# Optimization experiments

Hardware: AMD Instinct MI355X
Metric: run time of the kernel (lower is better)

The kernel has to match this reference:

```python
import jax, jax.numpy as jnp
import numpy as np

N_NODES = 100000


def setup_inputs() -> dict:
    key = jax.random.key(0)
    k1, k2, k3, k4 = jax.random.split(key, 4)
    x = jax.random.normal(k1, (N_NODES, 64), dtype=jnp.float32)
    W = jax.random.normal(k2, (64, 64), dtype=jnp.float32) * (1.0 / np.sqrt(64.0))
    src = jax.random.randint(k3, (1600000,), 0, N_NODES, dtype=jnp.int32)
    dst = jax.random.randint(k4, (1600000,), 0, N_NODES, dtype=jnp.int32)
    return {"x": x, "W": W, "src": src, "dst": dst}


def reference(x, W, src, dst):
    n = x.shape[0]
    ones = jnp.ones(src.shape[0], dtype=x.dtype)
    out_deg = jax.ops.segment_sum(ones, src, num_segments=n)  # out-degree of each node
    in_deg = jax.ops.segment_sum(ones, dst, num_segments=n)   # in-degree of each node
    norm_src = jnp.power(jnp.clip(out_deg, 1.0, None), -0.5)  # D_out^{-1/2}, clamp(min=1)
    norm_dst = jnp.power(jnp.clip(in_deg, 1.0, None), -0.5)   # D_in^{-1/2}, clamp(min=1)
    # in_feats == out_feats -> DGL aggregates first, then applies the weight
    feat = x * norm_src[:, None]                              # [N, d_in]
    msgs = feat[src]                                          # [E, d_in] gather
    agg = jax.ops.segment_sum(msgs, dst, num_segments=n)      # [N, d_in] scatter-add
    agg = agg * norm_dst[:, None]
    return agg @ W                                            # [N, d_out]
```

## Files before the change

### kernel.cpp

```cpp
#include <hip/hip_runtime.h>
#include <math.h>

#define D 64
#define SCAN_TILE 1024
#define SCAN_THREADS 256
#define SCAN_ITEMS 4
#define HS 16
#define BSHIFT 9
#define BW 512
#define CHUNK 8192

__device__ __forceinline__ unsigned pack_bf16(float a, float b) {
    unsigned ua = __float_as_uint(a);
    unsigned ub = __float_as_uint(b);
    ua = (ua + 0x7fffu + ((ua >> 16) & 1u)) >> 16;
    ub = (ub + 0x7fffu + ((ub >> 16) & 1u)) >> 16;
    return ua | (ub << 16);
}
__device__ __forceinline__ float blo(unsigned u) { return __uint_as_float(u << 16); }
__device__ __forceinline__ float bhi(unsigned u) { return __uint_as_float(u & 0xffff0000u); }


__global__ __launch_bounds__(256)
void bucket_count_chunks2_kernel(const int* __restrict__ src, const int* __restrict__ dst,
                                 int* __restrict__ bcnt_d, int* __restrict__ bcnt_s,
                                 int E, int NBv) {
    __shared__ int cd[256];
    __shared__ int cs[256];
    for (int i = threadIdx.x; i < NBv; i += 256) { cd[i] = 0; cs[i] = 0; }
    __syncthreads();
    int beg = blockIdx.x * CHUNK;
    int end = beg + CHUNK; if (end > E) end = E;
    for (int j = beg + threadIdx.x; j < end; j += 256) {
        atomicAdd(&cd[dst[j] >> BSHIFT], 1);
        atomicAdd(&cs[src[j] >> BSHIFT], 1);
    }
    __syncthreads();
    for (int i = threadIdx.x; i < NBv; i += 256) {
        bcnt_d[(size_t)blockIdx.x * NBv + i] = cd[i];
        bcnt_s[(size_t)blockIdx.x * NBv + i] = cs[i];
    }
}

__global__ __launch_bounds__(256)
void bucket_scan_chunks2_kernel(const int* __restrict__ bcnt_d, int* __restrict__ bstart_d,
                                int* __restrict__ btot_d,
                                const int* __restrict__ bcnt_s, int* __restrict__ bstart_s,
                                int* __restrict__ btot_s,
                                int nChunks, int NBv) {
    __shared__ int sdata[256];
    int which = (blockIdx.x >= NBv) ? 1 : 0;
    int b = blockIdx.x - which * NBv;
    const int* bcnt   = which ? bcnt_s : bcnt_d;
    int*       bstart = which ? bstart_s : bstart_d;
    int*       btot   = which ? btot_s : btot_d;
    int t = threadIdx.x;
    int carry = 0;
    for (int c0 = 0; c0 < nChunks; c0 += 256) {
        int c = c0 + t;
        int v = (c < nChunks) ? bcnt[(size_t)c * NBv + b] : 0;
        sdata[t] = v;
        __syncthreads();
        for (int off = 1; off < 256; off <<= 1) {
            int val = (t >= off) ? sdata[t - off] : 0;
            __syncthreads();
            if (t >= off) sdata[t] += val;
            __syncthreads();
        }
        if (c < nChunks) bstart[(size_t)c * NBv + b] = carry + sdata[t] - v;
        carry += sdata[255];
        __syncthreads();
    }
    if (t == 0) btot[b] = carry;
}

__global__ __launch_bounds__(256)
void bucket_base2_kernel(const int* __restrict__ btot_d, int* __restrict__ bbeg_d,
                         const int* __restrict__ btot_s, int* __restrict__ bbeg_s,
                         int NBv, int E) {
    __shared__ int sdata[256];
    const int* btot = (blockIdx.x == 0) ? btot_d : btot_s;
    int*       bbeg = (blockIdx.x == 0) ? bbeg_d : bbeg_s;
    int t = threadIdx.x;
    int v = (t < NBv) ? btot[t] : 0;
    sdata[t] = v;
    __syncthreads();
    for (int off = 1; off < 256; off <<= 1) {
        int val = (t >= off) ? sdata[t - off] : 0;
        __syncthreads();
        if (t >= off) sdata[t] += val;
        __syncthreads();
    }
    if (t < NBv) bbeg[t] = sdata[t] - v;
    if (t == 0) bbeg[NBv] = E;
}

__global__ __launch_bounds__(256)
void bucket_scatter2_kernel(const int* __restrict__ src, const int* __restrict__ dst,
                            const int* __restrict__ bstart_d, const int* __restrict__ bbeg_d,
                            const int* __restrict__ bstart_s, const int* __restrict__ bbeg_s,
                            unsigned* __restrict__ bucketed_d,
                            unsigned short* __restrict__ bucketed_s,
                            int E, int NBv) {
    __shared__ int cur_d[256];
    __shared__ int cur_s[256];
    for (int i = threadIdx.x; i < NBv; i += 256) {
        cur_d[i] = bstart_d[(size_t)blockIdx.x * NBv + i] + bbeg_d[i];
        cur_s[i] = bstart_s[(size_t)blockIdx.x * NBv + i] + bbeg_s[i];
    }
    __syncthreads();
    int beg = blockIdx.x * CHUNK;
    int end = beg + CHUNK; if (end > E) end = E;
    for (int j = beg + threadIdx.x; j < end; j += 256) {
        int d = dst[j];
        int s = src[j];
        int pd = atomicAdd(&cur_d[d >> BSHIFT], 1);
        bucketed_d[pd] = ((unsigned)(d & (BW - 1)) << 17) | (unsigned)s;
        int ps = atomicAdd(&cur_s[s >> BSHIFT], 1);
        bucketed_s[ps] = (unsigned short)(s & (BW - 1));
    }
}

__global__ __launch_bounds__(256)
void bucket_count_dst_kernel(const unsigned* __restrict__ bucketed_d,
                             const int* __restrict__ bbeg_d, int* __restrict__ cnt_dst,
                             float* __restrict__ norm_dst, int N) {
    __shared__ int cnt[BW];
    int b = blockIdx.x;
    for (int i = threadIdx.x; i < BW; i += 256) cnt[i] = 0;
    __syncthreads();
    int beg = bbeg_d[b], end = bbeg_d[b + 1];
    for (int j = beg + threadIdx.x; j < end; j += 256) {
        atomicAdd(&cnt[bucketed_d[j] >> 17], 1);
    }
    __syncthreads();
    int dbase = b << BSHIFT;
    for (int i = threadIdx.x; i < BW; i += 256) {
        int d = dbase + i;
        if (d < N) {
            int c = cnt[i];
            cnt_dst[d] = c;
            norm_dst[d] = 1.0f / sqrtf((float)(c < 1 ? 1 : c));
        }
    }
}

__global__ __launch_bounds__(256)
void bucket_count_src_kernel(const unsigned short* __restrict__ bucketed_s,
                             const int* __restrict__ bbeg_s, float* __restrict__ norm_src,
                             int N) {
    __shared__ int cnt[BW];
    int b = blockIdx.x;
    for (int i = threadIdx.x; i < BW; i += 256) cnt[i] = 0;
    __syncthreads();
    int beg = bbeg_s[b], end = bbeg_s[b + 1];
    for (int j = beg + threadIdx.x; j < end; j += 256) {
        atomicAdd(&cnt[bucketed_s[j]], 1);
    }
    __syncthreads();
    int sbase = b << BSHIFT;
    for (int i = threadIdx.x; i < BW; i += 256) {
        int s = sbase + i;
        if (s < N) {
            int c = cnt[i];
            norm_src[s] = 1.0f / sqrtf((float)(c < 1 ? 1 : c));
        }
    }
}

__global__ __launch_bounds__(256)
void bucket_place_kernel(const unsigned* __restrict__ bucketed_d,
                         const int* __restrict__ bbeg_d, const int* __restrict__ offsets,
                         int* __restrict__ sorted_src, int N) {
    __shared__ int cur[BW];
    int b = blockIdx.x;
    int dbase = b << BSHIFT;
    for (int i = threadIdx.x; i < BW; i += 256) {
        int d = dbase + i;
        cur[i] = (d < N) ? offsets[d] : 0;
    }
    __syncthreads();
    int beg = bbeg_d[b], end = bbeg_d[b + 1];
    for (int j = beg + threadIdx.x; j < end; j += 256) {
        unsigned v = bucketed_d[j];
        int pos = atomicAdd(&cur[v >> 17], 1);
        sorted_src[pos] = (int)(v & 0x1FFFFu);
    }
}


__global__ __launch_bounds__(SCAN_THREADS)
void scan_blocks_kernel(const int* __restrict__ cnt_dst, int* __restrict__ offsets,
                        int* __restrict__ partials, int N, int S) {
    __shared__ int sdata[SCAN_THREADS];
    int t = threadIdx.x;
    int base = blockIdx.x * SCAN_TILE + t * SCAN_ITEMS;
    int v[SCAN_ITEMS];
    int sum = 0;
    #pragma unroll
    for (int i = 0; i < SCAN_ITEMS; ++i) {
        int idx = base + i;
        v[i] = (idx < N) ? cnt_dst[(size_t)idx * S] : 0;
        sum += v[i];
    }
    sdata[t] = sum;
    __syncthreads();
    for (int off = 1; off < SCAN_THREADS; off <<= 1) {
        int val = (t >= off) ? sdata[t - off] : 0;
        __syncthreads();
        if (t >= off) sdata[t] += val;
        __syncthreads();
    }
    int excl = sdata[t] - sum;
    if (t == SCAN_THREADS - 1) partials[blockIdx.x] = sdata[t];
    int run = excl;
    #pragma unroll
    for (int i = 0; i < SCAN_ITEMS; ++i) {
        int idx = base + i;
        if (idx < N) offsets[idx] = run;
        run += v[i];
    }
}

__global__ __launch_bounds__(SCAN_THREADS)
void scan_partials_kernel(int* __restrict__ partials, int nblk) {
    __shared__ int sdata[SCAN_THREADS];
    int t = threadIdx.x;
    int v = (t < nblk) ? partials[t] : 0;
    sdata[t] = v;
    __syncthreads();
    for (int off = 1; off < SCAN_THREADS; off <<= 1) {
        int val = (t >= off) ? sdata[t - off] : 0;
        __syncthreads();
        if (t >= off) sdata[t] += val;
        __syncthreads();
    }
    if (t < nblk) partials[t] = sdata[t] - v;
}

__global__ void add_back2_kernel(int* __restrict__ offsets, const int* __restrict__ partials,
                                 int N, int E) {
    int i = blockIdx.x * blockDim.x + threadIdx.x;
    if (i < N) offsets[i] += partials[i >> 10];
    if (i == 0) offsets[N] = E;
}

__global__ void add_back_kernel(int* __restrict__ offsets, int* __restrict__ cursor,
                                const int* __restrict__ partials, int N, int E, int S) {
    int i = blockIdx.x * blockDim.x + threadIdx.x;
    if (i < N) {
        int o = offsets[i] + partials[i >> 10];
        offsets[i] = o;
        cursor[(size_t)i * S] = o;
    }
    if (i == 0) offsets[N] = E;
}


#define XW_ROWS 64
#define ATP 68

__global__ __launch_bounds__(256, 4)
void xw_tiled_kernel(const float4* __restrict__ x4, const float* __restrict__ W,
                     const float* __restrict__ norm_src, unsigned* __restrict__ y, int N) {
    __shared__ float Ws[D * D];
    __shared__ float At[D][ATP];
    int t = threadIdx.x;

    for (int i = t; i < D * D / 4; i += 256)
        reinterpret_cast<float4*>(Ws)[i] = reinterpret_cast<const float4*>(W)[i];

    int rowbase = blockIdx.x * XW_ROWS;
    int lr = t >> 2;
    int qc = t & 3;
    int gr = rowbase + lr;
    float ns = (gr < N) ? norm_src[gr] : 0.0f;
    #pragma unroll
    for (int c = qc; c < 16; c += 4) {
        float4 v = (gr < N) ? x4[(size_t)gr * 16 + c] : make_float4(0.f, 0.f, 0.f, 0.f);
        At[c * 4 + 0][lr] = v.x * ns;
        At[c * 4 + 1][lr] = v.y * ns;
        At[c * 4 + 2][lr] = v.z * ns;
        At[c * 4 + 3][lr] = v.w * ns;
    }
    __syncthreads();

    int tx = t & 15;
    int ty = t >> 4;
    float4 acc0 = make_float4(0.f, 0.f, 0.f, 0.f);
    float4 acc1 = acc0, acc2 = acc0, acc3 = acc0;
    #pragma unroll 4
    for (int k = 0; k < D; ++k) {
        float4 a = *reinterpret_cast<const float4*>(&At[k][ty * 4]);
        float4 w = *reinterpret_cast<const float4*>(&Ws[k * D + tx * 4]);
        acc0.x += a.x * w.x; acc0.y += a.x * w.y; acc0.z += a.x * w.z; acc0.w += a.x * w.w;
        acc1.x += a.y * w.x; acc1.y += a.y * w.y; acc1.z += a.y * w.z; acc1.w += a.y * w.w;
        acc2.x += a.z * w.x; acc2.y += a.z * w.y; acc2.z += a.z * w.z; acc2.w += a.z * w.w;
        acc3.x += a.w * w.x; acc3.y += a.w * w.y; acc3.z += a.w * w.z; acc3.w += a.w * w.w;
    }

    uint2* y2 = reinterpret_cast<uint2*>(y);
    int r0 = rowbase + ty * 4;
    if (r0 + 0 < N) y2[(size_t)(r0 + 0) * 16 + tx] =
        make_uint2(pack_bf16(acc0.x, acc0.y), pack_bf16(acc0.z, acc0.w));
    if (r0 + 1 < N) y2[(size_t)(r0 + 1) * 16 + tx] =
        make_uint2(pack_bf16(acc1.x, acc1.y), pack_bf16(acc1.z, acc1.w));
    if (r0 + 2 < N) y2[(size_t)(r0 + 2) * 16 + tx] =
        make_uint2(pack_bf16(acc2.x, acc2.y), pack_bf16(acc2.z, acc2.w));
    if (r0 + 3 < N) y2[(size_t)(r0 + 3) * 16 + tx] =
        make_uint2(pack_bf16(acc3.x, acc3.y), pack_bf16(acc3.z, acc3.w));
}


__global__ __launch_bounds__(256)
void agg_bf16_kernel(const uint4* __restrict__ y4, const int* __restrict__ offsets,
                     const int* __restrict__ sorted_src, const float* __restrict__ norm_dst,
                     float4* __restrict__ out4, int N) {
    int wave = (blockIdx.x << 2) + (threadIdx.x >> 6);
    if (wave >= N) return;
    int lane = threadIdx.x & 63;
    int g = lane >> 3;
    int q = lane & 7;
    int beg = offsets[wave];
    int end = offsets[wave + 1];
    float nd = norm_dst[wave];
    float a0 = 0.f, a1 = 0.f, a2 = 0.f, a3 = 0.f, a4 = 0.f, a5 = 0.f, a6 = 0.f, a7 = 0.f;
    int j = beg + g;
    while (j + 8 < end) {
        int s0 = sorted_src[j];
        int s1 = sorted_src[j + 8];
        uint4 v0 = y4[(size_t)s0 * 8 + q];
        uint4 v1 = y4[(size_t)s1 * 8 + q];
        a0 += blo(v0.x) + blo(v1.x); a1 += bhi(v0.x) + bhi(v1.x);
        a2 += blo(v0.y) + blo(v1.y); a3 += bhi(v0.y) + bhi(v1.y);
        a4 += blo(v0.z) + blo(v1.z); a5 += bhi(v0.z) + bhi(v1.z);
        a6 += blo(v0.w) + blo(v1.w); a7 += bhi(v0.w) + bhi(v1.w);
        j += 16;
    }
    if (j < end) {
        int s = sorted_src[j];
        uint4 v = y4[(size_t)s * 8 + q];
        a0 += blo(v.x); a1 += bhi(v.x);
        a2 += blo(v.y); a3 += bhi(v.y);
        a4 += blo(v.z); a5 += bhi(v.z);
        a6 += blo(v.w); a7 += bhi(v.w);
    }
    a0 += __shfl_xor(a0, 8);  a1 += __shfl_xor(a1, 8);
    a2 += __shfl_xor(a2, 8);  a3 += __shfl_xor(a3, 8);
    a4 += __shfl_xor(a4, 8);  a5 += __shfl_xor(a5, 8);
    a6 += __shfl_xor(a6, 8);  a7 += __shfl_xor(a7, 8);
    a0 += __shfl_xor(a0, 16); a1 += __shfl_xor(a1, 16);
    a2 += __shfl_xor(a2, 16); a3 += __shfl_xor(a3, 16);
    a4 += __shfl_xor(a4, 16); a5 += __shfl_xor(a5, 16);
    a6 += __shfl_xor(a6, 16); a7 += __shfl_xor(a7, 16);
    a0 += __shfl_xor(a0, 32); a1 += __shfl_xor(a1, 32);
    a2 += __shfl_xor(a2, 32); a3 += __shfl_xor(a3, 32);
    a4 += __shfl_xor(a4, 32); a5 += __shfl_xor(a5, 32);
    a6 += __shfl_xor(a6, 32); a7 += __shfl_xor(a7, 32);
    if (lane < 8) {
        float4 o1; o1.x = a0 * nd; o1.y = a1 * nd; o1.z = a2 * nd; o1.w = a3 * nd;
        float4 o2; o2.x = a4 * nd; o2.y = a5 * nd; o2.z = a6 * nd; o2.w = a7 * nd;
        out4[(size_t)wave * 16 + q * 2]     = o1;
        out4[(size_t)wave * 16 + q * 2 + 1] = o2;
    }
}


__global__ void hist4_kernel(const int* __restrict__ src, const int* __restrict__ dst,
                             int* __restrict__ cnt, int E, int N, int S) {
    int i = blockIdx.x * blockDim.x + threadIdx.x;
    int E4 = E >> 2;
    if (i < E4) {
        int4 s = reinterpret_cast<const int4*>(src)[i];
        int4 d = reinterpret_cast<const int4*>(dst)[i];
        atomicAdd(&cnt[s.x * S], 1); atomicAdd(&cnt[s.y * S], 1);
        atomicAdd(&cnt[s.z * S], 1); atomicAdd(&cnt[s.w * S], 1);
        atomicAdd(&cnt[(N + d.x) * S], 1); atomicAdd(&cnt[(N + d.y) * S], 1);
        atomicAdd(&cnt[(N + d.z) * S], 1); atomicAdd(&cnt[(N + d.w) * S], 1);
    }
    if (i == 0) {
        for (int e = E4 << 2; e < E; ++e) {
            atomicAdd(&cnt[src[e] * S], 1);
            atomicAdd(&cnt[(N + dst[e]) * S], 1);
        }
    }
}

__global__ void norm_from_cnt_kernel(const int* __restrict__ cnt, float* __restrict__ norm,
                                     int twoN, int S) {
    int i = blockIdx.x * blockDim.x + threadIdx.x;
    if (i < twoN) {
        int c = cnt[(size_t)i * S];
        float v = (float)(c < 1 ? 1 : c);
        norm[i] = 1.0f / sqrtf(v);
    }
}

__global__ void bin4_kernel(const int* __restrict__ src, const int* __restrict__ dst,
                            int* __restrict__ cursor, int* __restrict__ sorted_src,
                            int E, int S) {
    int i = blockIdx.x * blockDim.x + threadIdx.x;
    int E4 = E >> 2;
    if (i < E4) {
        int4 s = reinterpret_cast<const int4*>(src)[i];
        int4 d = reinterpret_cast<const int4*>(dst)[i];
        sorted_src[atomicAdd(&cursor[d.x * S], 1)] = s.x;
        sorted_src[atomicAdd(&cursor[d.y * S], 1)] = s.y;
        sorted_src[atomicAdd(&cursor[d.z * S], 1)] = s.z;
        sorted_src[atomicAdd(&cursor[d.w * S], 1)] = s.w;
    }
    if (i == 0) {
        for (int e = E4 << 2; e < E; ++e) {
            sorted_src[atomicAdd(&cursor[dst[e] * S], 1)] = src[e];
        }
    }
}

__global__ void deg_kernel(const int* __restrict__ src, const int* __restrict__ dst,
                           float* __restrict__ deg, int E, int N) {
    int i = blockIdx.x * blockDim.x + threadIdx.x;
    if (i < E) {
        atomicAdd(&deg[src[i]], 1.0f);
        atomicAdd(&deg[N + dst[i]], 1.0f);
    }
}

__global__ void norm_kernel(float* __restrict__ deg, int twoN) {
    int i = blockIdx.x * blockDim.x + threadIdx.x;
    if (i < twoN) {
        float v = deg[i];
        v = v < 1.0f ? 1.0f : v;
        deg[i] = 1.0f / sqrtf(v);
    }
}

__global__ void scatter_kernel(const float* __restrict__ x, const int* __restrict__ src,
                               const int* __restrict__ dst, const float* __restrict__ norm_src,
                               float* __restrict__ agg, int E) {
    int tid = blockIdx.x * blockDim.x + threadIdx.x;
    int e = tid >> 4;
    int q = tid & 15;
    if (e < E) {
        int s = src[e];
        int d = dst[e];
        float ns = norm_src[s];
        float4 v = reinterpret_cast<const float4*>(x)[s * (D / 4) + q];
        float* o = agg + (long long)d * D + q * 4;
        atomicAdd(o + 0, v.x * ns);
        atomicAdd(o + 1, v.y * ns);
        atomicAdd(o + 2, v.z * ns);
        atomicAdd(o + 3, v.w * ns);
    }
}

__global__ __launch_bounds__(256) void gemm_kernel(float* __restrict__ out,
                                                   const float* __restrict__ W,
                                                   const float* __restrict__ norm_dst,
                                                   int N, int rows_per_block) {
    __shared__ float Ws[D * D];
    __shared__ float rowS[4][D];
    for (int i = threadIdx.x; i < D * D; i += 256) Ws[i] = W[i];

    int f   = threadIdx.x & 63;
    int sub = threadIdx.x >> 6;
    int base = blockIdx.x * rows_per_block;

    for (int r0 = 0; r0 < rows_per_block; r0 += 4) {
        int r = base + r0 + sub;
        bool valid = (r < N);
        __syncthreads();
        if (valid) rowS[sub][f] = out[(long long)r * D + f] * norm_dst[r];
        __syncthreads();
        if (valid) {
            float acc = 0.0f;
            #pragma unroll
            for (int k = 0; k < D; ++k) acc += rowS[sub][k] * Ws[k * D + f];
            out[(long long)r * D + f] = acc;
        }
    }
}

extern "C" void kernel_launch(void* const* d_in, const int* in_sizes, int n_in,
                              void* d_out, int out_size, void* d_ws, size_t ws_size,
                              hipStream_t stream) {
    const float* x   = (const float*)d_in[0];
    const float* W   = (const float*)d_in[1];
    const int*   src = (const int*)d_in[2];
    const int*   dst = (const int*)d_in[3];

    const int N = in_sizes[0] / D;
    const int E = in_sizes[2];
    const int nblk = (N + SCAN_TILE - 1) / SCAN_TILE;
    const int NBv = (N + BW - 1) >> BSHIFT;
    const int nChunks = (E + CHUNK - 1) / CHUNK;

    size_t w_norm = 0;
    size_t w_cntd = w_norm + 2 * (size_t)N;
    size_t w_offs = w_cntd + (size_t)N;
    size_t w_part = w_offs + (size_t)N + 1;
    size_t w_bcd  = w_part + SCAN_THREADS;
    size_t w_bsd  = w_bcd + (size_t)nChunks * NBv;
    size_t w_bcs  = w_bsd + (size_t)nChunks * NBv;
    size_t w_bss  = w_bcs + (size_t)nChunks * NBv;
    size_t w_btd  = w_bss + (size_t)nChunks * NBv;
    size_t w_bbd  = w_btd + (size_t)NBv;
    size_t w_bts  = w_bbd + (size_t)NBv + 1;
    size_t w_bbs  = w_bts + (size_t)NBv;
    size_t w_bkd  = w_bbs + (size_t)NBv + 1;
    size_t w_bks  = w_bkd + (size_t)E;
    size_t w_sort = w_bks + ((size_t)E + 1) / 2;
    size_t w_y    = (w_sort + (size_t)E + 3) & ~(size_t)3;
    size_t need_new = (w_y + (size_t)N * 32) * 4;

    bool new_ok = (N <= (1 << 17)) && (NBv <= 256) && (nblk <= SCAN_THREADS) &&
                  (ws_size >= need_new);

    if (new_ok) {
        float*          norm       = (float*)d_ws + w_norm;
        int*            cnt_dst    = (int*)d_ws + w_cntd;
        int*            offsets    = (int*)d_ws + w_offs;
        int*            partials   = (int*)d_ws + w_part;
        int*            bcnt_d     = (int*)d_ws + w_bcd;
        int*            bstart_d   = (int*)d_ws + w_bsd;
        int*            bcnt_s     = (int*)d_ws + w_bcs;
        int*            bstart_s   = (int*)d_ws + w_bss;
        int*            btot_d     = (int*)d_ws + w_btd;
        int*            bbeg_d     = (int*)d_ws + w_bbd;
        int*            btot_s     = (int*)d_ws + w_bts;
        int*            bbeg_s     = (int*)d_ws + w_bbs;
        unsigned*       bucketed_d = (unsigned*)d_ws + w_bkd;
        unsigned short* bucketed_s = (unsigned short*)((int*)d_ws + w_bks);
        int*            sorted_src = (int*)d_ws + w_sort;
        unsigned*       y          = (unsigned*)d_ws + w_y;
        float*          out        = (float*)d_out;

        bucket_count_chunks2_kernel<<<nChunks, 256, 0, stream>>>(src, dst, bcnt_d, bcnt_s,
                                                                 E, NBv);
        bucket_scan_chunks2_kernel<<<2 * NBv, 256, 0, stream>>>(bcnt_d, bstart_d, btot_d,
                                                                bcnt_s, bstart_s, btot_s,
                                                                nChunks, NBv);
        bucket_base2_kernel<<<2, 256, 0, stream>>>(btot_d, bbeg_d, btot_s, bbeg_s, NBv, E);
        bucket_scatter2_kernel<<<nChunks, 256, 0, stream>>>(src, dst, bstart_d, bbeg_d,
                                                            bstart_s, bbeg_s, bucketed_d,
                                                            bucketed_s, E, NBv);
        bucket_count_src_kernel<<<NBv, 256, 0, stream>>>(bucketed_s, bbeg_s, norm, N);
        bucket_count_dst_kernel<<<NBv, 256, 0, stream>>>(bucketed_d, bbeg_d, cnt_dst,
                                                         norm + N, N);

        scan_blocks_kernel<<<nblk, SCAN_THREADS, 0, stream>>>(cnt_dst, offsets, partials, N, 1);
        scan_partials_kernel<<<1, SCAN_THREADS, 0, stream>>>(partials, nblk);
        add_back2_kernel<<<(N + 255) / 256, 256, 0, stream>>>(offsets, partials, N, E);

        bucket_place_kernel<<<NBv, 256, 0, stream>>>(bucketed_d, bbeg_d, offsets,
                                                     sorted_src, N);

        xw_tiled_kernel<<<(N + XW_ROWS - 1) / XW_ROWS, 256, 0, stream>>>(
            (const float4*)x, W, norm, y, N);
        int agg_blocks = (N + 3) / 4;
        agg_bf16_kernel<<<agg_blocks, 256, 0, stream>>>(
            (const uint4*)y, offsets, sorted_src, norm + N, (float4*)out, N);
        return;
    }

    {
        const int strides[4] = {16, 8, 4, 1};
        int S = 0;
        size_t o_norm = 0, o_cnt = 0, o_offs = 0, o_cur = 0, o_part = 0, o_sort = 0, o_yy = 0;
        size_t need_A = 0;
        for (int t = 0; t < 4; ++t) {
            int s = strides[t];
            o_norm = 0;
            o_cnt  = o_norm + 2 * (size_t)N;
            o_offs = o_cnt + 2 * (size_t)N * s;
            o_cur  = o_offs + (size_t)N + 1;
            o_part = o_cur + (size_t)N * s;
            o_sort = o_part + SCAN_THREADS;
            o_yy   = (o_sort + (size_t)E + 3) & ~(size_t)3;
            need_A = (o_yy + (size_t)N * 32) * 4;
            if (ws_size >= need_A) { S = s; break; }
        }
        if (S > 0 && nblk <= SCAN_THREADS) {
            float*    norm       = (float*)d_ws + o_norm;
            int*      cnt        = (int*)d_ws + o_cnt;
            int*      offsets    = (int*)d_ws + o_offs;
            int*      cursor     = (int*)d_ws + o_cur;
            int*      partials   = (int*)d_ws + o_part;
            int*      sorted_src = (int*)d_ws + o_sort;
            unsigned* y          = (unsigned*)d_ws + o_yy;
            float*    out        = (float*)d_out;

            hipMemsetAsync(cnt, 0, 2 * (size_t)N * S * sizeof(int), stream);

            int E4 = E >> 2;
            int histblk = (E4 + 255) / 256; if (histblk < 1) histblk = 1;
            hist4_kernel<<<histblk, 256, 0, stream>>>(src, dst, cnt, E, N, S);
            norm_from_cnt_kernel<<<(2 * N + 255) / 256, 256, 0, stream>>>(cnt, norm, 2 * N, S);
            scan_blocks_kernel<<<nblk, SCAN_THREADS, 0, stream>>>(cnt + (size_t)N * S, offsets,
                                                                  partials, N, S);
            scan_partials_kernel<<<1, SCAN_THREADS, 0, stream>>>(partials, nblk);
            add_back_kernel<<<(N + 255) / 256, 256, 0, stream>>>(offsets, cursor, partials,
                                                                 N, E, S);
            bin4_kernel<<<histblk, 256, 0, stream>>>(src, dst, cursor, sorted_src, E, S);

            xw_tiled_kernel<<<(N + XW_ROWS - 1) / XW_ROWS, 256, 0, stream>>>(
                (const float4*)x, W, norm, y, N);
            int agg_blocks = (N + 3) / 4;
            agg_bf16_kernel<<<agg_blocks, 256, 0, stream>>>(
                (const uint4*)y, offsets, sorted_src, norm + N, (float4*)out, N);
            return;
        }
    }

    {
        float* deg = (float*)d_ws;
        float* agg = (float*)d_out;

        hipMemsetAsync(deg, 0, (size_t)2 * N * sizeof(float), stream);
        hipMemsetAsync(agg, 0, (size_t)N * D * sizeof(float), stream);

        deg_kernel<<<(E + 255) / 256, 256, 0, stream>>>(src, dst, deg, E, N);
        norm_kernel<<<(2 * N + 255) / 256, 256, 0, stream>>>(deg, 2 * N);

        long long scatter_threads = (long long)E * 16;
        int scatter_blocks = (int)((scatter_threads + 255) / 256);
        scatter_kernel<<<scatter_blocks, 256, 0, stream>>>(x, src, dst, deg, agg, E);

        const int rows_per_block = 64;
        int gemm_blocks = (N + rows_per_block - 1) / rows_per_block;
        gemm_kernel<<<gemm_blocks, 256, 0, stream>>>(agg, W, deg + N, N, rows_per_block);
    }
}
```

Baseline: 155.2 us.

## Map eight lanes per destination row in aggregation instead of one wave

The aggregation kernel now gives each destination row 8 lanes (each loading one 16-byte bf16 slice), so a wave covers 8 rows instead of one. Each lane walks that row's edges serially, unrolled by 4, and the cross-lane shuffle reduction goes away. With about 16 edges per row, the old mapping left most lanes idle or needed a shuffle reduction at the end. In exchange, each lane runs a longer serial edge loop, and rows of different degree in the same wave cause divergence.

```diff
diff --git a/kernel.cpp b/kernel.cpp
--- a/kernel.cpp
+++ b/kernel.cpp
@@ -316,26 +316,43 @@
 void agg_bf16_kernel(const uint4* __restrict__ y4, const int* __restrict__ offsets,
                      const int* __restrict__ sorted_src, const float* __restrict__ norm_dst,
                      float4* __restrict__ out4, int N) {
-    int wave = (blockIdx.x << 2) + (threadIdx.x >> 6);
-    if (wave >= N) return;
-    int lane = threadIdx.x & 63;
-    int g = lane >> 3;
-    int q = lane & 7;
-    int beg = offsets[wave];
-    int end = offsets[wave + 1];
-    float nd = norm_dst[wave];
+    int row = blockIdx.x * 32 + (threadIdx.x >> 3);
+    if (row >= N) return;
+    int q = threadIdx.x & 7;
+    int beg = offsets[row];
+    int end = offsets[row + 1];
+    float nd = norm_dst[row];
     float a0 = 0.f, a1 = 0.f, a2 = 0.f, a3 = 0.f, a4 = 0.f, a5 = 0.f, a6 = 0.f, a7 = 0.f;
-    int j = beg + g;
-    while (j + 8 < end) {
+    int j = beg;
+    while (j + 3 < end) {
         int s0 = sorted_src[j];
-        int s1 = sorted_src[j + 8];
+        int s1 = sorted_src[j + 1];
+        int s2 = sorted_src[j + 2];
+        int s3 = sorted_src[j + 3];
+        uint4 v0 = y4[(size_t)s0 * 8 + q];
+        uint4 v1 = y4[(size_t)s1 * 8 + q];
+        uint4 v2 = y4[(size_t)s2 * 8 + q];
+        uint4 v3 = y4[(size_t)s3 * 8 + q];
+        a0 += (blo(v0.x) + blo(v1.x)) + (blo(v2.x) + blo(v3.x));
+        a1 += (bhi(v0.x) + bhi(v1.x)) + (bhi(v2.x) + bhi(v3.x));
+        a2 += (blo(v0.y) + blo(v1.y)) + (blo(v2.y) + blo(v3.y));
+        a3 += (bhi(v0.y) + bhi(v1.y)) + (bhi(v2.y) + bhi(v3.y));
+        a4 += (blo(v0.z) + blo(v1.z)) + (blo(v2.z) + blo(v3.z));
+        a5 += (bhi(v0.z) + bhi(v1.z)) + (bhi(v2.z) + bhi(v3.z));
+        a6 += (blo(v0.w) + blo(v1.w)) + (blo(v2.w) + blo(v3.w));
+        a7 += (bhi(v0.w) + bhi(v1.w)) + (bhi(v2.w) + bhi(v3.w));
+        j += 4;
+    }
+    if (j + 1 < end) {
+        int s0 = sorted_src[j];
+        int s1 = sorted_src[j + 1];
         uint4 v0 = y4[(size_t)s0 * 8 + q];
         uint4 v1 = y4[(size_t)s1 * 8 + q];
         a0 += blo(v0.x) + blo(v1.x); a1 += bhi(v0.x) + bhi(v1.x);
         a2 += blo(v0.y) + blo(v1.y); a3 += bhi(v0.y) + bhi(v1.y);
         a4 += blo(v0.z) + blo(v1.z); a5 += bhi(v0.z) + bhi(v1.z);
         a6 += blo(v0.w) + blo(v1.w); a7 += bhi(v0.w) + bhi(v1.w);
-        j += 16;
+        j += 2;
     }
     if (j < end) {
         int s = sorted_src[j];
@@ -345,24 +362,10 @@
         a4 += blo(v.z); a5 += bhi(v.z);
         a6 += blo(v.w); a7 += bhi(v.w);
     }
-    a0 += __shfl_xor(a0, 8);  a1 += __shfl_xor(a1, 8);
-    a2 += __shfl_xor(a2, 8);  a3 += __shfl_xor(a3, 8);
-    a4 += __shfl_xor(a4, 8);  a5 += __shfl_xor(a5, 8);
-    a6 += __shfl_xor(a6, 8);  a7 += __shfl_xor(a7, 8);
-    a0 += __shfl_xor(a0, 16); a1 += __shfl_xor(a1, 16);
-    a2 += __shfl_xor(a2, 16); a3 += __shfl_xor(a3, 16);
-    a4 += __shfl_xor(a4, 16); a5 += __shfl_xor(a5, 16);
-    a6 += __shfl_xor(a6, 16); a7 += __shfl_xor(a7, 16);
-    a0 += __shfl_xor(a0, 32); a1 += __shfl_xor(a1, 32);
-    a2 += __shfl_xor(a2, 32); a3 += __shfl_xor(a3, 32);
-    a4 += __shfl_xor(a4, 32); a5 += __shfl_xor(a5, 32);
-    a6 += __shfl_xor(a6, 32); a7 += __shfl_xor(a7, 32);
-    if (lane < 8) {
-        float4 o1; o1.x = a0 * nd; o1.y = a1 * nd; o1.z = a2 * nd; o1.w = a3 * nd;
-        float4 o2; o2.x = a4 * nd; o2.y = a5 * nd; o2.z = a6 * nd; o2.w = a7 * nd;
-        out4[(size_t)wave * 16 + q * 2]     = o1;
-        out4[(size_t)wave * 16 + q * 2 + 1] = o2;
-    }
+    float4 o1; o1.x = a0 * nd; o1.y = a1 * nd; o1.z = a2 * nd; o1.w = a3 * nd;
+    float4 o2; o2.x = a4 * nd; o2.y = a5 * nd; o2.z = a6 * nd; o2.w = a7 * nd;
+    out4[(size_t)row * 16 + q * 2]     = o1;
+    out4[(size_t)row * 16 + q * 2 + 1] = o2;
 }
 
 
@@ -556,7 +559,7 @@
 
         xw_tiled_kernel<<<(N + XW_ROWS - 1) / XW_ROWS, 256, 0, stream>>>(
             (const float4*)x, W, norm, y, N);
-        int agg_blocks = (N + 3) / 4;
+        int agg_blocks = (N + 31) / 32;
         agg_bf16_kernel<<<agg_blocks, 256, 0, stream>>>(
             (const uint4*)y, offsets, sorted_src, norm + N, (float4*)out, N);
         return;
@@ -604,7 +607,7 @@
 
             xw_tiled_kernel<<<(N + XW_ROWS - 1) / XW_ROWS, 256, 0, stream>>>(
                 (const float4*)x, W, norm, y, N);
-            int agg_blocks = (N + 3) / 4;
+            int agg_blocks = (N + 31) / 32;
             agg_bf16_kernel<<<agg_blocks, 256, 0, stream>>>(
                 (const uint4*)y, offsets, sorted_src, norm + N, (float4*)out, N);
             return;
```

Measured after the change: 157.3 us. Within noise of the previous version (+1.4%).

## Fuse degree count, CSR offset scan and placement into one bucket kernel

Applied to the files above, without the earlier changes.

Replaces the separate src/dst count kernels, the three-kernel global prefix scan, and the placement kernel with a single finalize kernel. Because buckets are already laid out contiguously by destination range, each block derives its node offsets from the bucket base plus a local block scan, so no global scan is needed. It also shrinks CHUNK from 8192 to 2048 to give the count and scatter stages more blocks. This cuts five kernel launches and one global pass over the counts, but grows the per-chunk bucket count tables and the bucket-scan work.

```diff
diff --git a/kernel.cpp b/kernel.cpp
--- a/kernel.cpp
+++ b/kernel.cpp
@@ -8,7 +8,7 @@
 #define HS 16
 #define BSHIFT 9
 #define BW 512
-#define CHUNK 8192
+#define CHUNK 2048
 
 __device__ __forceinline__ unsigned pack_bf16(float a, float b) {
     unsigned ua = __float_as_uint(a);
@@ -122,69 +122,71 @@
 }
 
 __global__ __launch_bounds__(256)
-void bucket_count_dst_kernel(const unsigned* __restrict__ bucketed_d,
-                             const int* __restrict__ bbeg_d, int* __restrict__ cnt_dst,
-                             float* __restrict__ norm_dst, int N) {
+void bucket_finalize_kernel(const unsigned* __restrict__ bucketed_d,
+                            const int* __restrict__ bbeg_d,
+                            const unsigned short* __restrict__ bucketed_s,
+                            const int* __restrict__ bbeg_s,
+                            int* __restrict__ offsets, float* __restrict__ norm_dst,
+                            float* __restrict__ norm_src, int* __restrict__ sorted_src,
+                            int N, int E, int NBv) {
     __shared__ int cnt[BW];
-    int b = blockIdx.x;
-    for (int i = threadIdx.x; i < BW; i += 256) cnt[i] = 0;
-    __syncthreads();
-    int beg = bbeg_d[b], end = bbeg_d[b + 1];
-    for (int j = beg + threadIdx.x; j < end; j += 256) {
-        atomicAdd(&cnt[bucketed_d[j] >> 17], 1);
-    }
-    __syncthreads();
-    int dbase = b << BSHIFT;
-    for (int i = threadIdx.x; i < BW; i += 256) {
-        int d = dbase + i;
-        if (d < N) {
-            int c = cnt[i];
-            cnt_dst[d] = c;
-            norm_dst[d] = 1.0f / sqrtf((float)(c < 1 ? 1 : c));
-        }
-    }
-}
-
-__global__ __launch_bounds__(256)
-void bucket_count_src_kernel(const unsigned short* __restrict__ bucketed_s,
-                             const int* __restrict__ bbeg_s, float* __restrict__ norm_src,
-                             int N) {
-    __shared__ int cnt[BW];
-    int b = blockIdx.x;
-    for (int i = threadIdx.x; i < BW; i += 256) cnt[i] = 0;
-    __syncthreads();
-    int beg = bbeg_s[b], end = bbeg_s[b + 1];
-    for (int j = beg + threadIdx.x; j < end; j += 256) {
-        atomicAdd(&cnt[bucketed_s[j]], 1);
-    }
-    __syncthreads();
-    int sbase = b << BSHIFT;
-    for (int i = threadIdx.x; i < BW; i += 256) {
-        int s = sbase + i;
-        if (s < N) {
-            int c = cnt[i];
-            norm_src[s] = 1.0f / sqrtf((float)(c < 1 ? 1 : c));
-        }
-    }
-}
-
-__global__ __launch_bounds__(256)
-void bucket_place_kernel(const unsigned* __restrict__ bucketed_d,
-                         const int* __restrict__ bbeg_d, const int* __restrict__ offsets,
-                         int* __restrict__ sorted_src, int N) {
     __shared__ int cur[BW];
-    int b = blockIdx.x;
-    int dbase = b << BSHIFT;
-    for (int i = threadIdx.x; i < BW; i += 256) {
-        int d = dbase + i;
-        cur[i] = (d < N) ? offsets[d] : 0;
-    }
-    __syncthreads();
-    int beg = bbeg_d[b], end = bbeg_d[b + 1];
-    for (int j = beg + threadIdx.x; j < end; j += 256) {
-        unsigned v = bucketed_d[j];
-        int pos = atomicAdd(&cur[v >> 17], 1);
-        sorted_src[pos] = (int)(v & 0x1FFFFu);
+    __shared__ int ssum[256];
+    int t = threadIdx.x;
+    if (blockIdx.x < NBv) {
+        int b = blockIdx.x;
+        cnt[t] = 0; cnt[t + 256] = 0;
+        __syncthreads();
+        int beg = bbeg_d[b], end = bbeg_d[b + 1];
+        for (int j = beg + t; j < end; j += 256)
+            atomicAdd(&cnt[bucketed_d[j] >> 17], 1);
+        __syncthreads();
+        int c0 = cnt[2 * t], c1 = cnt[2 * t + 1];
+        ssum[t] = c0 + c1;
+        __syncthreads();
+        for (int off = 1; off < 256; off <<= 1) {
+            int v = (t >= off) ? ssum[t - off] : 0;
+            __syncthreads();
+            if (t >= off) ssum[t] += v;
+            __syncthreads();
+        }
+        int excl = ssum[t] - (c0 + c1);
+        int off0 = beg + excl;
+        int off1 = off0 + c0;
+        int dbase = b << BSHIFT;
+        int d0 = dbase + 2 * t, d1 = dbase + 2 * t + 1;
+        cur[2 * t] = off0; cur[2 * t + 1] = off1;
+        if (d0 < N) {
+            offsets[d0] = off0;
+            norm_dst[d0] = 1.0f / sqrtf((float)(c0 < 1 ? 1 : c0));
+        }
+        if (d1 < N) {
+            offsets[d1] = off1;
+            norm_dst[d1] = 1.0f / sqrtf((float)(c1 < 1 ? 1 : c1));
+        }
+        if (b == NBv - 1 && t == 0) offsets[N] = E;
+        __syncthreads();
+        for (int j = beg + t; j < end; j += 256) {
+            unsigned v = bucketed_d[j];
+            int pos = atomicAdd(&cur[v >> 17], 1);
+            sorted_src[pos] = (int)(v & 0x1FFFFu);
+        }
+    } else {
+        int b = blockIdx.x - NBv;
+        cnt[t] = 0; cnt[t + 256] = 0;
+        __syncthreads();
+        int beg = bbeg_s[b], end = bbeg_s[b + 1];
+        for (int j = beg + t; j < end; j += 256)
+            atomicAdd(&cnt[bucketed_s[j]], 1);
+        __syncthreads();
+        int sbase = b << BSHIFT;
+        for (int i = t; i < BW; i += 256) {
+            int s = sbase + i;
+            if (s < N) {
+                int c = cnt[i];
+                norm_src[s] = 1.0f / sqrtf((float)(c < 1 ? 1 : c));
+            }
+        }
     }
 }
 
@@ -236,13 +238,6 @@
         __syncthreads();
     }
     if (t < nblk) partials[t] = sdata[t] - v;
-}
-
-__global__ void add_back2_kernel(int* __restrict__ offsets, const int* __restrict__ partials,
-                                 int N, int E) {
-    int i = blockIdx.x * blockDim.x + threadIdx.x;
-    if (i < N) offsets[i] += partials[i >> 10];
-    if (i == 0) offsets[N] = E;
 }
 
 __global__ void add_back_kernel(int* __restrict__ offsets, int* __restrict__ cursor,
@@ -495,10 +490,8 @@
     const int nChunks = (E + CHUNK - 1) / CHUNK;
 
     size_t w_norm = 0;
-    size_t w_cntd = w_norm + 2 * (size_t)N;
-    size_t w_offs = w_cntd + (size_t)N;
-    size_t w_part = w_offs + (size_t)N + 1;
-    size_t w_bcd  = w_part + SCAN_THREADS;
+    size_t w_offs = w_norm + 2 * (size_t)N;
+    size_t w_bcd  = w_offs + (size_t)N + 1;
     size_t w_bsd  = w_bcd + (size_t)nChunks * NBv;
     size_t w_bcs  = w_bsd + (size_t)nChunks * NBv;
     size_t w_bss  = w_bcs + (size_t)nChunks * NBv;
@@ -512,14 +505,11 @@
     size_t w_y    = (w_sort + (size_t)E + 3) & ~(size_t)3;
     size_t need_new = (w_y + (size_t)N * 32) * 4;
 
-    bool new_ok = (N <= (1 << 17)) && (NBv <= 256) && (nblk <= SCAN_THREADS) &&
-                  (ws_size >= need_new);
+    bool new_ok = (N <= (1 << 17)) && (NBv <= 256) && (ws_size >= need_new);
 
     if (new_ok) {
         float*          norm       = (float*)d_ws + w_norm;
-        int*            cnt_dst    = (int*)d_ws + w_cntd;
         int*            offsets    = (int*)d_ws + w_offs;
-        int*            partials   = (int*)d_ws + w_part;
         int*            bcnt_d     = (int*)d_ws + w_bcd;
         int*            bstart_d   = (int*)d_ws + w_bsd;
         int*            bcnt_s     = (int*)d_ws + w_bcs;
@@ -543,16 +533,10 @@
         bucket_scatter2_kernel<<<nChunks, 256, 0, stream>>>(src, dst, bstart_d, bbeg_d,
                                                             bstart_s, bbeg_s, bucketed_d,
                                                             bucketed_s, E, NBv);
-        bucket_count_src_kernel<<<NBv, 256, 0, stream>>>(bucketed_s, bbeg_s, norm, N);
-        bucket_count_dst_kernel<<<NBv, 256, 0, stream>>>(bucketed_d, bbeg_d, cnt_dst,
-                                                         norm + N, N);
-
-        scan_blocks_kernel<<<nblk, SCAN_THREADS, 0, stream>>>(cnt_dst, offsets, partials, N, 1);
-        scan_partials_kernel<<<1, SCAN_THREADS, 0, stream>>>(partials, nblk);
-        add_back2_kernel<<<(N + 255) / 256, 256, 0, stream>>>(offsets, partials, N, E);
-
-        bucket_place_kernel<<<NBv, 256, 0, stream>>>(bucketed_d, bbeg_d, offsets,
-                                                     sorted_src, N);
+        bucket_finalize_kernel<<<2 * NBv, 256, 0, stream>>>(bucketed_d, bbeg_d,
+                                                            bucketed_s, bbeg_s,
+                                                            offsets, norm + N, norm,
+                                                            sorted_src, N, E, NBv);
 
         xw_tiled_kernel<<<(N + XW_ROWS - 1) / XW_ROWS, 256, 0, stream>>>(
             (const float4*)x, W, norm, y, N);
```

New measurement: 142.7 us. 1.09x faster.
